# Optimization experiments

Measured on AMD Instinct MI355X. Metric: run time of the kernel, lower is better.

The kernel has to match this reference:

```python
import jax, jax.numpy as jnp
import numpy as np

N_NODES = 50000
N_EDGES = 20000
EDGE_SIZE = 32
IN_CH = 256
OUT_CH = 256


def setup_inputs() -> dict:
    key = jax.random.key(0)
    k1, k2, k3 = jax.random.split(key, 3)
    x = jax.random.normal(k1, (N_NODES, IN_CH), dtype=jnp.float32)
    hyperedges = jax.random.randint(k2, (N_EDGES, EDGE_SIZE), 0, N_NODES)
    weight = jax.random.normal(k3, (IN_CH, OUT_CH), dtype=jnp.float32)
    return {"x": x, "hyperedges": hyperedges, "weight": weight}


def reference(x, hyperedges, weight):
    # Gather node features per hyperedge and reduce ('sum' aggregation):
    # [E, K, C] -> [E, C]
    edge_sum = x[hyperedges].sum(axis=1)
    # Scatter-add each hyperedge's summed feature back to every member node.
    agg = jnp.zeros_like(x).at[hyperedges].add(edge_sum[:, None, :])
    # Dense projection + ReLU.
    return jax.nn.relu(agg @ weight)
```

## Files before the change

kernel.cpp:

```cpp
#include <hip/hip_runtime.h>
#include <hip/hip_bf16.h>

#define N_NODES 50000
#define N_EDGES 20000
#define EDGE_K  32
#define CH      256
#define N_INC   (N_EDGES * EDGE_K)
#define ELL_CAP 64

typedef __attribute__((ext_vector_type(4))) float f32x4;
typedef __attribute__((ext_vector_type(8))) short bf16x8;

static __device__ __forceinline__ unsigned short f2bf(float f) {
    __hip_bfloat16 h = __float2bfloat16(f);
    return *reinterpret_cast<unsigned short*>(&h);
}

static __device__ __forceinline__ float bf2f(unsigned short u) {
    unsigned int b = ((unsigned int)u) << 16;
    float f;
    __builtin_memcpy(&f, &b, 4);
    return f;
}

#define CONV_BLOCKS ((N_NODES * CH / 4 + 255) / 256)
#define ZERO_BLOCKS ((N_NODES + 255) / 256)
__global__ void prep_kernel(const float* __restrict__ x, unsigned short* __restrict__ xb,
                            const float* __restrict__ w, unsigned short* __restrict__ wt,
                            int* __restrict__ deg) {
    int b = blockIdx.x;
    if (b < CONV_BLOCKS) {
        int i = b * 256 + threadIdx.x;
        if (i < N_NODES * CH / 4) {
            f32x4 v = reinterpret_cast<const f32x4*>(x)[i];
            ushort4 s;
            s.x = f2bf(v.x);
            s.y = f2bf(v.y);
            s.z = f2bf(v.z);
            s.w = f2bf(v.w);
            reinterpret_cast<ushort4*>(xb)[i] = s;
        }
    } else if (b < CONV_BLOCKS + CH) {
        int n = b - CONV_BLOCKS;
        int k = threadIdx.x;
        wt[n * CH + k] = f2bf(w[k * CH + n]);
    } else {
        int i = (b - CONV_BLOCKS - CH) * 256 + threadIdx.x;
        if (i < N_NODES) deg[i] = 0;
    }
}

#define FILL_GROUPS   8
#define NODES_PER_GRP (N_NODES / FILL_GROUPS)
#define FILL_WIN      2560
#define FILL_BLOCKS   ((N_INC / FILL_WIN) * FILL_GROUPS)
#define GATHER_BLOCKS ((N_EDGES + 3) / 4)
__global__ void gather_fill_kernel(const unsigned short* __restrict__ xb,
                                   const int* __restrict__ he,
                                   unsigned short* __restrict__ es,
                                   int* __restrict__ deg,
                                   unsigned short* __restrict__ ell) {
    int b = blockIdx.x;
    if (b < FILL_BLOCKS) {
        int g  = b % FILL_GROUPS;
        int wn = b / FILL_GROUPS;
        int lo = g * NODES_PER_GRP, hi = lo + NODES_PER_GRP;
        int base = wn * FILL_WIN;
#pragma unroll
        for (int it = 0; it < FILL_WIN / 256; ++it) {
            int i = base + it * 256 + threadIdx.x;
            int node = he[i];
            if (node >= lo && node < hi) {
                int slot = atomicAdd(&deg[node], 1);
                if (slot < ELL_CAP)
                    ell[(size_t)node * ELL_CAP + slot] = (unsigned short)(i >> 5);
            }
        }
    } else {
        int wave = (b - FILL_BLOCKS) * 4 + (threadIdx.x >> 6);
        int lane = threadIdx.x & 63;
        if (wave >= N_EDGES) return;
        int myidx = he[wave * EDGE_K + (lane & 31)];
        const ushort4* xb4 = reinterpret_cast<const ushort4*>(xb);
        f32x4 acc = {0.f, 0.f, 0.f, 0.f};
#pragma unroll
        for (int k = 0; k < EDGE_K; ++k) {
            int e = __shfl(myidx, k, 64);
            ushort4 v = xb4[(size_t)e * (CH / 4) + lane];
            acc.x += bf2f(v.x);
            acc.y += bf2f(v.y);
            acc.z += bf2f(v.z);
            acc.w += bf2f(v.w);
        }
        ushort4 s;
        s.x = f2bf(acc.x);
        s.y = f2bf(acc.y);
        s.z = f2bf(acc.z);
        s.w = f2bf(acc.w);
        reinterpret_cast<ushort4*>(es + (size_t)wave * CH)[lane] = s;
    }
}

__global__ __launch_bounds__(256) void gemm_kernel(const unsigned short* __restrict__ es,
                                                   const unsigned short* __restrict__ wt,
                                                   unsigned short* __restrict__ yb) {
    int wid  = threadIdx.x >> 6;
    int lane = threadIdx.x & 63;
    int m0   = blockIdx.x * 64 + wid * 16;
    if (m0 >= N_EDGES) return;
    int lr = lane & 15;
    int lg = lane >> 4;

    f32x4 acc[16] = {};

    const unsigned short* arow = es + (size_t)(m0 + lr) * CH + lg * 8;
#pragma unroll
    for (int kk = 0; kk < CH; kk += 32) {
        bf16x8 a = *reinterpret_cast<const bf16x8*>(arow + kk);
#pragma unroll
        for (int nt = 0; nt < 16; ++nt) {
            bf16x8 b = *reinterpret_cast<const bf16x8*>(
                wt + (size_t)(nt * 16 + lr) * CH + kk + lg * 8);
            acc[nt] = __builtin_amdgcn_mfma_f32_16x16x32_bf16(a, b, acc[nt], 0, 0, 0);
        }
    }

#pragma unroll
    for (int nt = 0; nt < 16; ++nt) {
#pragma unroll
        for (int r = 0; r < 4; ++r) {
            yb[(size_t)(m0 + lg * 4 + r) * CH + nt * 16 + lr] = f2bf(acc[nt][r]);
        }
    }
}

__global__ void apply_kernel(const unsigned short* __restrict__ yb, const int* __restrict__ deg,
                             const unsigned short* __restrict__ ell, float* __restrict__ out) {
    int node = (int)((blockIdx.x * blockDim.x + threadIdx.x) >> 6);
    int lane = threadIdx.x & 63;
    if (node >= N_NODES) return;
    int d = deg[node];
    if (d > ELL_CAP) d = ELL_CAP;
    int myidx = (int)ell[(size_t)node * ELL_CAP + lane];
    const ushort4* yb4 = reinterpret_cast<const ushort4*>(yb);
    f32x4 acc = {0.f, 0.f, 0.f, 0.f};
    int j = 0;
    for (; j + 4 <= d; j += 4) {
        int e0 = __shfl(myidx, j + 0, 64);
        int e1 = __shfl(myidx, j + 1, 64);
        int e2 = __shfl(myidx, j + 2, 64);
        int e3 = __shfl(myidx, j + 3, 64);
        ushort4 v0 = yb4[(size_t)e0 * (CH / 4) + lane];
        ushort4 v1 = yb4[(size_t)e1 * (CH / 4) + lane];
        ushort4 v2 = yb4[(size_t)e2 * (CH / 4) + lane];
        ushort4 v3 = yb4[(size_t)e3 * (CH / 4) + lane];
        acc.x += bf2f(v0.x) + bf2f(v1.x) + bf2f(v2.x) + bf2f(v3.x);
        acc.y += bf2f(v0.y) + bf2f(v1.y) + bf2f(v2.y) + bf2f(v3.y);
        acc.z += bf2f(v0.z) + bf2f(v1.z) + bf2f(v2.z) + bf2f(v3.z);
        acc.w += bf2f(v0.w) + bf2f(v1.w) + bf2f(v2.w) + bf2f(v3.w);
    }
    for (; j < d; ++j) {
        int e = __shfl(myidx, j, 64);
        ushort4 v = yb4[(size_t)e * (CH / 4) + lane];
        acc.x += bf2f(v.x);
        acc.y += bf2f(v.y);
        acc.z += bf2f(v.z);
        acc.w += bf2f(v.w);
    }
    acc.x = fmaxf(acc.x, 0.f);
    acc.y = fmaxf(acc.y, 0.f);
    acc.z = fmaxf(acc.z, 0.f);
    acc.w = fmaxf(acc.w, 0.f);
    reinterpret_cast<f32x4*>(out + (size_t)node * CH)[lane] = acc;
}

extern "C" void kernel_launch(void* const* d_in, const int* in_sizes, int n_in,
                              void* d_out, int out_size, void* d_ws, size_t ws_size,
                              hipStream_t stream) {
    const float* x  = (const float*)d_in[0];
    const int*   he = (const int*)d_in[1];
    const float* w  = (const float*)d_in[2];
    float* out = (float*)d_out;

    char* ws = (char*)d_ws;
    unsigned short* wt  = (unsigned short*)ws;
    unsigned short* es  = (unsigned short*)(ws + 131072);
    unsigned short* yb  = (unsigned short*)(ws + 131072 + 10240000);
    int* deg = (int*)(ws + 131072 + 10240000 + 10240000);
    unsigned short* ell = (unsigned short*)(ws + 131072 + 10240000 + 10240000 + 200000);

    unsigned short* xb = (unsigned short*)d_out;

    prep_kernel<<<CONV_BLOCKS + CH + ZERO_BLOCKS, 256, 0, stream>>>(x, xb, w, wt, deg);

    gather_fill_kernel<<<FILL_BLOCKS + GATHER_BLOCKS, 256, 0, stream>>>(xb, he, es, deg, ell);

    {
        int blocks = (N_EDGES + 63) / 64;
        gemm_kernel<<<blocks, 256, 0, stream>>>(es, wt, yb);
    }

    {
        int blocks = (N_NODES + 3) / 4;
        apply_kernel<<<blocks, 256, 0, stream>>>(yb, deg, ell, out);
    }
}
```

Before: 158.5 us.

## Fuse hyperedge gather with MFMA projection via shared-memory tile

Merges the per-hyperedge gather-sum and the bf16 MFMA GEMM into one kernel. Each block gathers 16 edge sums into padded shared memory, then its four waves each compute four 16-column output tiles. This drops the intermediate es buffer round-trip through global memory and removes one kernel launch. It also unrolls the apply kernel's gather to 8 loads in flight. In exchange, each block reloads the full weight matrix from cache, and the gather is serialized as 4 edges per wave before the barrier.

```diff
diff --git a/kernel.cpp b/kernel.cpp
--- a/kernel.cpp
+++ b/kernel.cpp
@@ -54,12 +54,12 @@
 #define NODES_PER_GRP (N_NODES / FILL_GROUPS)
 #define FILL_WIN      2560
 #define FILL_BLOCKS   ((N_INC / FILL_WIN) * FILL_GROUPS)
-#define GATHER_BLOCKS ((N_EDGES + 3) / 4)
-__global__ void gather_fill_kernel(const unsigned short* __restrict__ xb,
-                                   const int* __restrict__ he,
-                                   unsigned short* __restrict__ es,
-                                   int* __restrict__ deg,
-                                   unsigned short* __restrict__ ell) {
+#define GG_BLOCKS     (N_EDGES / 16)
+#define ZPAD          264
+__global__ __launch_bounds__(256) void gather_fill_gemm_kernel(
+        const unsigned short* __restrict__ xb, const int* __restrict__ he,
+        const unsigned short* __restrict__ wt, unsigned short* __restrict__ yb,
+        int* __restrict__ deg, unsigned short* __restrict__ ell) {
     int b = blockIdx.x;
     if (b < FILL_BLOCKS) {
         int g  = b % FILL_GROUPS;
@@ -76,17 +76,23 @@
                     ell[(size_t)node * ELL_CAP + slot] = (unsigned short)(i >> 5);
             }
         }
-    } else {
-        int wave = (b - FILL_BLOCKS) * 4 + (threadIdx.x >> 6);
-        int lane = threadIdx.x & 63;
-        if (wave >= N_EDGES) return;
-        int myidx = he[wave * EDGE_K + (lane & 31)];
-        const ushort4* xb4 = reinterpret_cast<const ushort4*>(xb);
+        return;
+    }
+
+    __shared__ unsigned short zs[16 * ZPAD];
+    int w    = threadIdx.x >> 6;
+    int lane = threadIdx.x & 63;
+    int ebase = (b - FILL_BLOCKS) * 16;
+
+    const ushort4* xb4 = reinterpret_cast<const ushort4*>(xb);
+    for (int t = 0; t < 4; ++t) {
+        int e = ebase + w * 4 + t;
+        int myidx = he[e * EDGE_K + (lane & 31)];
         f32x4 acc = {0.f, 0.f, 0.f, 0.f};
 #pragma unroll
         for (int k = 0; k < EDGE_K; ++k) {
-            int e = __shfl(myidx, k, 64);
-            ushort4 v = xb4[(size_t)e * (CH / 4) + lane];
+            int idx = __shfl(myidx, k, 64);
+            ushort4 v = xb4[(size_t)idx * (CH / 4) + lane];
             acc.x += bf2f(v.x);
             acc.y += bf2f(v.y);
             acc.z += bf2f(v.z);
@@ -97,39 +103,28 @@
         s.y = f2bf(acc.y);
         s.z = f2bf(acc.z);
         s.w = f2bf(acc.w);
-        reinterpret_cast<ushort4*>(es + (size_t)wave * CH)[lane] = s;
-    }
-}
-
-__global__ __launch_bounds__(256) void gemm_kernel(const unsigned short* __restrict__ es,
-                                                   const unsigned short* __restrict__ wt,
-                                                   unsigned short* __restrict__ yb) {
-    int wid  = threadIdx.x >> 6;
-    int lane = threadIdx.x & 63;
-    int m0   = blockIdx.x * 64 + wid * 16;
-    if (m0 >= N_EDGES) return;
+        *reinterpret_cast<ushort4*>(&zs[(w * 4 + t) * ZPAD + lane * 4]) = s;
+    }
+    __syncthreads();
+
     int lr = lane & 15;
     int lg = lane >> 4;
-
-    f32x4 acc[16] = {};
-
-    const unsigned short* arow = es + (size_t)(m0 + lr) * CH + lg * 8;
+    f32x4 acc[4] = {};
 #pragma unroll
     for (int kk = 0; kk < CH; kk += 32) {
-        bf16x8 a = *reinterpret_cast<const bf16x8*>(arow + kk);
-#pragma unroll
-        for (int nt = 0; nt < 16; ++nt) {
-            bf16x8 b = *reinterpret_cast<const bf16x8*>(
-                wt + (size_t)(nt * 16 + lr) * CH + kk + lg * 8);
-            acc[nt] = __builtin_amdgcn_mfma_f32_16x16x32_bf16(a, b, acc[nt], 0, 0, 0);
-        }
-    }
-
-#pragma unroll
-    for (int nt = 0; nt < 16; ++nt) {
+        bf16x8 a = *reinterpret_cast<const bf16x8*>(&zs[lr * ZPAD + kk + lg * 8]);
+#pragma unroll
+        for (int nt = 0; nt < 4; ++nt) {
+            bf16x8 bb = *reinterpret_cast<const bf16x8*>(
+                wt + (size_t)((w * 4 + nt) * 16 + lr) * CH + kk + lg * 8);
+            acc[nt] = __builtin_amdgcn_mfma_f32_16x16x32_bf16(a, bb, acc[nt], 0, 0, 0);
+        }
+    }
+#pragma unroll
+    for (int nt = 0; nt < 4; ++nt) {
 #pragma unroll
         for (int r = 0; r < 4; ++r) {
-            yb[(size_t)(m0 + lg * 4 + r) * CH + nt * 16 + lr] = f2bf(acc[nt][r]);
+            yb[(size_t)(ebase + lg * 4 + r) * CH + (w * 4 + nt) * 16 + lr] = f2bf(acc[nt][r]);
         }
     }
 }
@@ -145,23 +140,36 @@
     const ushort4* yb4 = reinterpret_cast<const ushort4*>(yb);
     f32x4 acc = {0.f, 0.f, 0.f, 0.f};
     int j = 0;
+    for (; j + 8 <= d; j += 8) {
+        ushort4 v0 = yb4[(size_t)__shfl(myidx, j + 0, 64) * (CH / 4) + lane];
+        ushort4 v1 = yb4[(size_t)__shfl(myidx, j + 1, 64) * (CH / 4) + lane];
+        ushort4 v2 = yb4[(size_t)__shfl(myidx, j + 2, 64) * (CH / 4) + lane];
+        ushort4 v3 = yb4[(size_t)__shfl(myidx, j + 3, 64) * (CH / 4) + lane];
+        ushort4 v4 = yb4[(size_t)__shfl(myidx, j + 4, 64) * (CH / 4) + lane];
+        ushort4 v5 = yb4[(size_t)__shfl(myidx, j + 5, 64) * (CH / 4) + lane];
+        ushort4 v6 = yb4[(size_t)__shfl(myidx, j + 6, 64) * (CH / 4) + lane];
+        ushort4 v7 = yb4[(size_t)__shfl(myidx, j + 7, 64) * (CH / 4) + lane];
+        acc.x += bf2f(v0.x) + bf2f(v1.x) + bf2f(v2.x) + bf2f(v3.x)
+               + bf2f(v4.x) + bf2f(v5.x) + bf2f(v6.x) + bf2f(v7.x);
+        acc.y += bf2f(v0.y) + bf2f(v1.y) + bf2f(v2.y) + bf2f(v3.y)
+               + bf2f(v4.y) + bf2f(v5.y) + bf2f(v6.y) + bf2f(v7.y);
+        acc.z += bf2f(v0.z) + bf2f(v1.z) + bf2f(v2.z) + bf2f(v3.z)
+               + bf2f(v4.z) + bf2f(v5.z) + bf2f(v6.z) + bf2f(v7.z);
+        acc.w += bf2f(v0.w) + bf2f(v1.w) + bf2f(v2.w) + bf2f(v3.w)
+               + bf2f(v4.w) + bf2f(v5.w) + bf2f(v6.w) + bf2f(v7.w);
+    }
     for (; j + 4 <= d; j += 4) {
-        int e0 = __shfl(myidx, j + 0, 64);
-        int e1 = __shfl(myidx, j + 1, 64);
-        int e2 = __shfl(myidx, j + 2, 64);
-        int e3 = __shfl(myidx, j + 3, 64);
-        ushort4 v0 = yb4[(size_t)e0 * (CH / 4) + lane];
-        ushort4 v1 = yb4[(size_t)e1 * (CH / 4) + lane];
-        ushort4 v2 = yb4[(size_t)e2 * (CH / 4) + lane];
-        ushort4 v3 = yb4[(size_t)e3 * (CH / 4) + lane];
+        ushort4 v0 = yb4[(size_t)__shfl(myidx, j + 0, 64) * (CH / 4) + lane];
+        ushort4 v1 = yb4[(size_t)__shfl(myidx, j + 1, 64) * (CH / 4) + lane];
+        ushort4 v2 = yb4[(size_t)__shfl(myidx, j + 2, 64) * (CH / 4) + lane];
+        ushort4 v3 = yb4[(size_t)__shfl(myidx, j + 3, 64) * (CH / 4) + lane];
         acc.x += bf2f(v0.x) + bf2f(v1.x) + bf2f(v2.x) + bf2f(v3.x);
         acc.y += bf2f(v0.y) + bf2f(v1.y) + bf2f(v2.y) + bf2f(v3.y);
         acc.z += bf2f(v0.z) + bf2f(v1.z) + bf2f(v2.z) + bf2f(v3.z);
         acc.w += bf2f(v0.w) + bf2f(v1.w) + bf2f(v2.w) + bf2f(v3.w);
     }
     for (; j < d; ++j) {
-        int e = __shfl(myidx, j, 64);
-        ushort4 v = yb4[(size_t)e * (CH / 4) + lane];
+        ushort4 v = yb4[(size_t)__shfl(myidx, j, 64) * (CH / 4) + lane];
         acc.x += bf2f(v.x);
         acc.y += bf2f(v.y);
         acc.z += bf2f(v.z);
@@ -184,21 +192,16 @@
 
     char* ws = (char*)d_ws;
     unsigned short* wt  = (unsigned short*)ws;
-    unsigned short* es  = (unsigned short*)(ws + 131072);
-    unsigned short* yb  = (unsigned short*)(ws + 131072 + 10240000);
-    int* deg = (int*)(ws + 131072 + 10240000 + 10240000);
-    unsigned short* ell = (unsigned short*)(ws + 131072 + 10240000 + 10240000 + 200000);
+    unsigned short* yb  = (unsigned short*)(ws + 131072);
+    int* deg = (int*)(ws + 131072 + 10240000);
+    unsigned short* ell = (unsigned short*)(ws + 131072 + 10240000 + 200000);
 
     unsigned short* xb = (unsigned short*)d_out;
 
     prep_kernel<<<CONV_BLOCKS + CH + ZERO_BLOCKS, 256, 0, stream>>>(x, xb, w, wt, deg);
 
-    gather_fill_kernel<<<FILL_BLOCKS + GATHER_BLOCKS, 256, 0, stream>>>(xb, he, es, deg, ell);
-
-    {
-        int blocks = (N_EDGES + 63) / 64;
-        gemm_kernel<<<blocks, 256, 0, stream>>>(es, wt, yb);
-    }
+    gather_fill_gemm_kernel<<<FILL_BLOCKS + GG_BLOCKS, 256, 0, stream>>>(
+        xb, he, wt, yb, deg, ell);
 
     {
         int blocks = (N_NODES + 3) / 4;
```

Result: faster. 146.7 us (-7.5%).

## Slice feature channels into 8 planes for cache-local gathers and scatters

Applied to the files above, without the earlier changes.

The bf16 node features and the projected edge rows are now stored channel-sliced: 8 planes of 32 channels, each plane contiguous across nodes or edges. Gather and apply blocks each work on one slice, so the random-access working set per slice is one eighth the size and more likely to stay in L2/MALL. Each wave now handles 4 edges or nodes, with lanes split across members and channels and a cross-lane shuffle reduction at the end. In exchange there are 8x more blocks, a per-block reduction step, and predicated loads in the degree loop of the apply kernel.

```diff
diff --git a/kernel.cpp b/kernel.cpp
--- a/kernel.cpp
+++ b/kernel.cpp
@@ -7,6 +7,8 @@
 #define CH      256
 #define N_INC   (N_EDGES * EDGE_K)
 #define ELL_CAP 64
+#define NSLICE  8
+#define SCH     32
 
 typedef __attribute__((ext_vector_type(4))) float f32x4;
 typedef __attribute__((ext_vector_type(8))) short bf16x8;
@@ -15,15 +17,19 @@
     __hip_bfloat16 h = __float2bfloat16(f);
     return *reinterpret_cast<unsigned short*>(&h);
 }
-
-static __device__ __forceinline__ float bf2f(unsigned short u) {
-    unsigned int b = ((unsigned int)u) << 16;
-    float f;
-    __builtin_memcpy(&f, &b, 4);
-    return f;
-}
-
-#define CONV_BLOCKS ((N_NODES * CH / 4 + 255) / 256)
+static __device__ __forceinline__ float bflo(unsigned int u) {
+    unsigned int b = u << 16;
+    float f; __builtin_memcpy(&f, &b, 4); return f;
+}
+static __device__ __forceinline__ float bfhi(unsigned int u) {
+    unsigned int b = u & 0xffff0000u;
+    float f; __builtin_memcpy(&f, &b, 4); return f;
+}
+static __device__ __forceinline__ unsigned int pk2(float a, float b) {
+    return (unsigned int)f2bf(a) | ((unsigned int)f2bf(b) << 16);
+}
+
+#define CONV_BLOCKS (N_NODES * CH / 8 / 256)
 #define ZERO_BLOCKS ((N_NODES + 255) / 256)
 __global__ void prep_kernel(const float* __restrict__ x, unsigned short* __restrict__ xb,
                             const float* __restrict__ w, unsigned short* __restrict__ wt,
@@ -31,15 +37,17 @@
     int b = blockIdx.x;
     if (b < CONV_BLOCKS) {
         int i = b * 256 + threadIdx.x;
-        if (i < N_NODES * CH / 4) {
-            f32x4 v = reinterpret_cast<const f32x4*>(x)[i];
-            ushort4 s;
-            s.x = f2bf(v.x);
-            s.y = f2bf(v.y);
-            s.z = f2bf(v.z);
-            s.w = f2bf(v.w);
-            reinterpret_cast<ushort4*>(xb)[i] = s;
-        }
+        int n = i >> 5, sub = i & 31;
+        int g = sub >> 2, cp = (sub & 3) * 8;
+        const float* src = x + (size_t)n * CH + sub * 8;
+        f32x4 v0 = *reinterpret_cast<const f32x4*>(src);
+        f32x4 v1 = *reinterpret_cast<const f32x4*>(src + 4);
+        uint4 u;
+        u.x = pk2(v0.x, v0.y);
+        u.y = pk2(v0.z, v0.w);
+        u.z = pk2(v1.x, v1.y);
+        u.w = pk2(v1.z, v1.w);
+        *reinterpret_cast<uint4*>(xb + ((size_t)g * N_NODES + n) * SCH + cp) = u;
     } else if (b < CONV_BLOCKS + CH) {
         int n = b - CONV_BLOCKS;
         int k = threadIdx.x;
@@ -54,12 +62,12 @@
 #define NODES_PER_GRP (N_NODES / FILL_GROUPS)
 #define FILL_WIN      2560
 #define FILL_BLOCKS   ((N_INC / FILL_WIN) * FILL_GROUPS)
-#define GATHER_BLOCKS ((N_EDGES + 3) / 4)
-__global__ void gather_fill_kernel(const unsigned short* __restrict__ xb,
-                                   const int* __restrict__ he,
-                                   unsigned short* __restrict__ es,
-                                   int* __restrict__ deg,
-                                   unsigned short* __restrict__ ell) {
+#define GGRP          (N_EDGES / 16)
+#define GATHER_BLOCKS (GGRP * NSLICE)
+__global__ __launch_bounds__(256) void gather_fill_kernel(
+        const unsigned short* __restrict__ xb, const int* __restrict__ he,
+        unsigned short* __restrict__ es, int* __restrict__ deg,
+        unsigned short* __restrict__ ell) {
     int b = blockIdx.x;
     if (b < FILL_BLOCKS) {
         int g  = b % FILL_GROUPS;
@@ -76,28 +84,40 @@
                     ell[(size_t)node * ELL_CAP + slot] = (unsigned short)(i >> 5);
             }
         }
-    } else {
-        int wave = (b - FILL_BLOCKS) * 4 + (threadIdx.x >> 6);
-        int lane = threadIdx.x & 63;
-        if (wave >= N_EDGES) return;
-        int myidx = he[wave * EDGE_K + (lane & 31)];
-        const ushort4* xb4 = reinterpret_cast<const ushort4*>(xb);
-        f32x4 acc = {0.f, 0.f, 0.f, 0.f};
-#pragma unroll
-        for (int k = 0; k < EDGE_K; ++k) {
-            int e = __shfl(myidx, k, 64);
-            ushort4 v = xb4[(size_t)e * (CH / 4) + lane];
-            acc.x += bf2f(v.x);
-            acc.y += bf2f(v.y);
-            acc.z += bf2f(v.z);
-            acc.w += bf2f(v.w);
-        }
-        ushort4 s;
-        s.x = f2bf(acc.x);
-        s.y = f2bf(acc.y);
-        s.z = f2bf(acc.z);
-        s.w = f2bf(acc.w);
-        reinterpret_cast<ushort4*>(es + (size_t)wave * CH)[lane] = s;
+        return;
+    }
+    int gb  = b - FILL_BLOCKS;
+    int g   = gb & 7;
+    int grp = gb >> 3;
+    int w = threadIdx.x >> 6, lane = threadIdx.x & 63;
+    int ebase = grp * 16 + w * 4;
+    const int* hp = he + (size_t)ebase * EDGE_K;
+    int s = lane & 15;
+    int ep = lane >> 4, k = (lane >> 2) & 3, q = lane & 3;
+    int mA = hp[ep * 32 + s];
+    int mB = hp[ep * 32 + 16 + s];
+    const unsigned short* xg = xb + (size_t)g * N_NODES * SCH;
+    float a[8] = {0.f, 0.f, 0.f, 0.f, 0.f, 0.f, 0.f, 0.f};
+#pragma unroll
+    for (int r = 0; r < 8; ++r) {
+        int e = __shfl((r < 4) ? mA : mB, (lane & 48) + ((r * 4 + k) & 15), 64);
+        uint4 d = *reinterpret_cast<const uint4*>(xg + (size_t)e * SCH + q * 8);
+        a[0] += bflo(d.x); a[1] += bfhi(d.x);
+        a[2] += bflo(d.y); a[3] += bfhi(d.y);
+        a[4] += bflo(d.z); a[5] += bfhi(d.z);
+        a[6] += bflo(d.w); a[7] += bfhi(d.w);
+    }
+#pragma unroll
+    for (int j = 0; j < 8; ++j) a[j] += __shfl_xor(a[j], 4, 64);
+#pragma unroll
+    for (int j = 0; j < 8; ++j) a[j] += __shfl_xor(a[j], 8, 64);
+    if ((lane & 12) == 0) {
+        uint4 u;
+        u.x = pk2(a[0], a[1]);
+        u.y = pk2(a[2], a[3]);
+        u.z = pk2(a[4], a[5]);
+        u.w = pk2(a[6], a[7]);
+        *reinterpret_cast<uint4*>(es + (size_t)(ebase + ep) * CH + g * SCH + q * 8) = u;
     }
 }
 
@@ -112,66 +132,78 @@
     int lg = lane >> 4;
 
     f32x4 acc[16] = {};
-
     const unsigned short* arow = es + (size_t)(m0 + lr) * CH + lg * 8;
 #pragma unroll
     for (int kk = 0; kk < CH; kk += 32) {
         bf16x8 a = *reinterpret_cast<const bf16x8*>(arow + kk);
 #pragma unroll
         for (int nt = 0; nt < 16; ++nt) {
-            bf16x8 b = *reinterpret_cast<const bf16x8*>(
+            bf16x8 bb = *reinterpret_cast<const bf16x8*>(
                 wt + (size_t)(nt * 16 + lr) * CH + kk + lg * 8);
-            acc[nt] = __builtin_amdgcn_mfma_f32_16x16x32_bf16(a, b, acc[nt], 0, 0, 0);
-        }
-    }
-
+            acc[nt] = __builtin_amdgcn_mfma_f32_16x16x32_bf16(a, bb, acc[nt], 0, 0, 0);
+        }
+    }
 #pragma unroll
     for (int nt = 0; nt < 16; ++nt) {
 #pragma unroll
         for (int r = 0; r < 4; ++r) {
-            yb[(size_t)(m0 + lg * 4 + r) * CH + nt * 16 + lr] = f2bf(acc[nt][r]);
-        }
-    }
-}
-
-__global__ void apply_kernel(const unsigned short* __restrict__ yb, const int* __restrict__ deg,
-                             const unsigned short* __restrict__ ell, float* __restrict__ out) {
-    int node = (int)((blockIdx.x * blockDim.x + threadIdx.x) >> 6);
-    int lane = threadIdx.x & 63;
-    if (node >= N_NODES) return;
+            int row = m0 + lg * 4 + r;
+            yb[((size_t)(nt >> 1) * N_EDGES + row) * SCH + (nt & 1) * 16 + lr] =
+                f2bf(acc[nt][r]);
+        }
+    }
+}
+
+#define AP_NPB    16
+#define AP_BLOCKS ((N_NODES / AP_NPB) * NSLICE)
+__global__ __launch_bounds__(256) void apply_kernel(
+        const unsigned short* __restrict__ yb, const int* __restrict__ deg,
+        const unsigned short* __restrict__ ell, float* __restrict__ out) {
+    int b = blockIdx.x;
+    int g = b & 7;
+    int w = threadIdx.x >> 6, lane = threadIdx.x & 63;
+    int np = lane >> 4, s = lane & 15, k = (lane >> 2) & 3, q = lane & 3;
+    int node = (b >> 3) * AP_NPB + w * 4 + np;
     int d = deg[node];
     if (d > ELL_CAP) d = ELL_CAP;
-    int myidx = (int)ell[(size_t)node * ELL_CAP + lane];
-    const ushort4* yb4 = reinterpret_cast<const ushort4*>(yb);
-    f32x4 acc = {0.f, 0.f, 0.f, 0.f};
-    int j = 0;
-    for (; j + 4 <= d; j += 4) {
-        int e0 = __shfl(myidx, j + 0, 64);
-        int e1 = __shfl(myidx, j + 1, 64);
-        int e2 = __shfl(myidx, j + 2, 64);
-        int e3 = __shfl(myidx, j + 3, 64);
-        ushort4 v0 = yb4[(size_t)e0 * (CH / 4) + lane];
-        ushort4 v1 = yb4[(size_t)e1 * (CH / 4) + lane];
-        ushort4 v2 = yb4[(size_t)e2 * (CH / 4) + lane];
-        ushort4 v3 = yb4[(size_t)e3 * (CH / 4) + lane];
-        acc.x += bf2f(v0.x) + bf2f(v1.x) + bf2f(v2.x) + bf2f(v3.x);
-        acc.y += bf2f(v0.y) + bf2f(v1.y) + bf2f(v2.y) + bf2f(v3.y);
-        acc.z += bf2f(v0.z) + bf2f(v1.z) + bf2f(v2.z) + bf2f(v3.z);
-        acc.w += bf2f(v0.w) + bf2f(v1.w) + bf2f(v2.w) + bf2f(v3.w);
-    }
-    for (; j < d; ++j) {
-        int e = __shfl(myidx, j, 64);
-        ushort4 v = yb4[(size_t)e * (CH / 4) + lane];
-        acc.x += bf2f(v.x);
-        acc.y += bf2f(v.y);
-        acc.z += bf2f(v.z);
-        acc.w += bf2f(v.w);
-    }
-    acc.x = fmaxf(acc.x, 0.f);
-    acc.y = fmaxf(acc.y, 0.f);
-    acc.z = fmaxf(acc.z, 0.f);
-    acc.w = fmaxf(acc.w, 0.f);
-    reinterpret_cast<f32x4*>(out + (size_t)node * CH)[lane] = acc;
+    const unsigned short* er = ell + (size_t)node * ELL_CAP;
+    int m0 = er[s], m1 = er[16 + s], m2 = er[32 + s], m3 = er[48 + s];
+    int dmax = d;
+    dmax = max(dmax, __shfl_xor(dmax, 16, 64));
+    dmax = max(dmax, __shfl_xor(dmax, 32, 64));
+    const unsigned short* yg = yb + (size_t)g * N_EDGES * SCH;
+    float a[8] = {0.f, 0.f, 0.f, 0.f, 0.f, 0.f, 0.f, 0.f};
+#pragma unroll
+    for (int rq = 0; rq < 4; ++rq) {
+        if (rq * 16 >= dmax) break;
+        int m = (rq == 0) ? m0 : (rq == 1) ? m1 : (rq == 2) ? m2 : m3;
+#pragma unroll
+        for (int rr = 0; rr < 4; ++rr) {
+            int slot = rq * 16 + rr * 4 + k;
+            int e = __shfl(m, (lane & 48) + rr * 4 + k, 64);
+            if (slot < d) {
+                uint4 dd = *reinterpret_cast<const uint4*>(yg + (size_t)e * SCH + q * 8);
+                a[0] += bflo(dd.x); a[1] += bfhi(dd.x);
+                a[2] += bflo(dd.y); a[3] += bfhi(dd.y);
+                a[4] += bflo(dd.z); a[5] += bfhi(dd.z);
+                a[6] += bflo(dd.w); a[7] += bfhi(dd.w);
+            }
+        }
+    }
+#pragma unroll
+    for (int j = 0; j < 8; ++j) a[j] += __shfl_xor(a[j], 4, 64);
+#pragma unroll
+    for (int j = 0; j < 8; ++j) a[j] += __shfl_xor(a[j], 8, 64);
+    if ((lane & 12) == 0) {
+        f32x4 r0, r1;
+        r0.x = fmaxf(a[0], 0.f); r0.y = fmaxf(a[1], 0.f);
+        r0.z = fmaxf(a[2], 0.f); r0.w = fmaxf(a[3], 0.f);
+        r1.x = fmaxf(a[4], 0.f); r1.y = fmaxf(a[5], 0.f);
+        r1.z = fmaxf(a[6], 0.f); r1.w = fmaxf(a[7], 0.f);
+        float* dst = out + (size_t)node * CH + g * SCH + q * 8;
+        *reinterpret_cast<f32x4*>(dst)     = r0;
+        *reinterpret_cast<f32x4*>(dst + 4) = r1;
+    }
 }
 
 extern "C" void kernel_launch(void* const* d_in, const int* in_sizes, int n_in,
@@ -200,8 +232,5 @@
         gemm_kernel<<<blocks, 256, 0, stream>>>(es, wt, yb);
     }
 
-    {
-        int blocks = (N_NODES + 3) / 4;
-        apply_kernel<<<blocks, 256, 0, stream>>>(yb, deg, ell, out);
-    }
-}
+    apply_kernel<<<AP_BLOCKS, 256, 0, stream>>>(yb, deg, ell, out);
+}
```

After: 145.4 us. 8.3% less time.
